# Kernel tuning notes

Measured on AMD Instinct MI355X. Metric: run time of the kernel, lower is better.

Reference implementation:

```python
import jax, jax.numpy as jnp
import numpy as np
import math

D_MODEL = 1024
D_STATE = 16
D_CONV = 4
EXPAND = 2
D_INNER = EXPAND * D_MODEL
DT_RANK = 64
BATCH = 4
SEQ_LEN = 2048


def setup_inputs() -> dict:
    key = jax.random.key(0)
    ks = jax.random.split(key, 10)
    hidden_states = jax.random.normal(ks[0], (BATCH, SEQ_LEN, D_MODEL), jnp.float32)
    in_proj_w = jax.random.normal(ks[1], (D_MODEL, 2 * D_INNER), jnp.float32) * (D_MODEL ** -0.5)
    conv_w = jax.random.normal(ks[2], (D_INNER, D_CONV), jnp.float32) * (D_CONV ** -0.5)
    conv_b = jnp.zeros((D_INNER,), jnp.float32)
    x_proj_w = jax.random.normal(ks[3], (D_INNER, DT_RANK + 2 * D_STATE), jnp.float32) * (D_INNER ** -0.5)
    dt_init_std = DT_RANK ** -0.5
    dt_proj_w = jax.random.uniform(ks[4], (DT_RANK, D_INNER), jnp.float32, -dt_init_std, dt_init_std)
    # inverse-softplus init of dt bias: dt ~ logUniform(dt_min, dt_max)
    dt_min, dt_max, dt_floor = 0.001, 0.1, 1e-4
    dt = jnp.exp(jax.random.uniform(ks[5], (D_INNER,), jnp.float32) * (math.log(dt_max) - math.log(dt_min)) + math.log(dt_min))
    dt = jnp.clip(dt, dt_floor, None)
    dt_proj_b = dt + jnp.log(-jnp.expm1(-dt))
    A = jnp.tile(jnp.arange(1, D_STATE + 1, dtype=jnp.float32)[None, :], (D_INNER, 1))
    A_log = jnp.log(A)
    D = jnp.ones((D_INNER,), jnp.float32)
    out_proj_w = jax.random.normal(ks[6], (D_INNER, D_MODEL), jnp.float32) * (D_INNER ** -0.5)
    return {
        "hidden_states": hidden_states,
        "in_proj_w": in_proj_w,
        "conv_w": conv_w,
        "conv_b": conv_b,
        "x_proj_w": x_proj_w,
        "dt_proj_w": dt_proj_w,
        "dt_proj_b": dt_proj_b,
        "A_log": A_log,
        "D": D,
        "out_proj_w": out_proj_w,
    }


def _mamba_forward(hidden_states, in_proj_w, conv_w, conv_b, x_proj_w, dt_proj_w, dt_proj_b, A_log, D, out_proj_w):
    b, L, _ = hidden_states.shape
    d_state = A_log.shape[1]
    dt_rank = dt_proj_w.shape[0]
    K = conv_w.shape[1]

    xz = hidden_states @ in_proj_w                     # (b, L, 2*d_inner)
    x, z = jnp.split(xz, 2, axis=-1)                   # each (b, L, d_inner)

    # causal depthwise conv1d (padding = K-1, truncated to L)
    x_pad = jnp.pad(x, ((0, 0), (K - 1, 0), (0, 0)))
    x = sum(x_pad[:, k:k + L, :] * conv_w[:, k] for k in range(K)) + conv_b
    x = jax.nn.silu(x)

    x_dbl = x @ x_proj_w                               # (b, L, dt_rank + 2*d_state)
    dt, B, C = jnp.split(x_dbl, [dt_rank, dt_rank + d_state], axis=-1)
    dt = jax.nn.softplus(dt @ dt_proj_w + dt_proj_b)   # (b, L, d_inner)
    A = -jnp.exp(A_log)                                # (d_inner, d_state)

    def step(h, inp):
        x_t, dt_t, B_t, C_t = inp                      # (b,d), (b,d), (b,n), (b,n)
        dA = jnp.exp(A[None] * dt_t[..., None])        # (b, d, n)
        h = dA * h + dt_t[..., None] * B_t[:, None, :] * x_t[..., None]
        y_t = jnp.einsum('bdn,bn->bd', h, C_t) + D * x_t
        return h, y_t

    h0 = jnp.zeros((b, x.shape[-1], d_state), x.dtype)
    xs = (x.transpose(1, 0, 2), dt.transpose(1, 0, 2), B.transpose(1, 0, 2), C.transpose(1, 0, 2))
    _, ys = jax.lax.scan(step, h0, xs)                 # ys: (L, b, d_inner)
    y = ys.transpose(1, 0, 2) * jax.nn.silu(z)
    return y @ out_proj_w                              # (b, L, d_model)


def reference(hidden_states, in_proj_w, conv_w, conv_b, x_proj_w, dt_proj_w, dt_proj_b, A_log, D, out_proj_w):
    return _mamba_forward(hidden_states, in_proj_w, conv_w, conv_b, x_proj_w, dt_proj_w, dt_proj_b, A_log, D, out_proj_w)
```

## Files before the change

### kernel.cpp

```cpp
#include <hip/hip_runtime.h>
#include <hip/hip_bf16.h>


#define DM 1024
#define DS 16
#define DC 4
#define DI 2048
#define DR 64
#define NB 4
#define SL 2048
#define NTOK (NB*SL)
#define XDBL_W (DR + 2*DS)
#define CONV_R 8

typedef __hip_bfloat16 bf16;
typedef unsigned short u16;
typedef __attribute__((ext_vector_type(8))) short s8v;
typedef __attribute__((ext_vector_type(4))) float f4v;
typedef __attribute__((ext_vector_type(2))) float f2v;
typedef __attribute__((ext_vector_type(4))) unsigned short us4;

__device__ __forceinline__ float b2f(bf16 v) { return __bfloat162float(v); }
__device__ __forceinline__ bf16  f2b(float v) { return __float2bfloat16(v); }
__device__ __forceinline__ u16 f2u(float x) {
    union { bf16 h; u16 s; } u; u.h = f2b(x); return u.s;
}
__device__ __forceinline__ float u2f(u16 s) {
    union { bf16 h; u16 s; } u; u.s = s; return b2f(u.h);
}

__device__ __forceinline__ bool sniff_bf16(const void* Dones) {
    return ((const u16*)Dones)[0] == 0x3F80u;
}

__device__ __forceinline__ float softplus_fast(float v) {
    return fmaxf(v, 0.f) + __logf(1.f + __expf(-fabsf(v)));
}

__device__ __forceinline__ float silu_fast(float v) {
    return v * __builtin_amdgcn_rcpf(1.f + __expf(-v));
}

template<int MODE>
__device__ __forceinline__ float ld(const void* p, size_t i, bool bf) {
    if (MODE == 0) return b2f(((const bf16*)p)[i]);
    if (MODE == 1) return ((const float*)p)[i];
    return bf ? b2f(((const bf16*)p)[i]) : ((const float*)p)[i];
}
template<int MODE>
__device__ __forceinline__ void st(void* p, size_t i, bool bf, float v) {
    if (MODE == 0)      { ((bf16*)p)[i] = f2b(v); }
    else if (MODE == 1) { ((float*)p)[i] = v; }
    else { if (bf) ((bf16*)p)[i] = f2b(v); else ((float*)p)[i] = v; }
}

template<int CM>
__device__ __forceinline__ void cstore(void* C, void* C2, size_t m, int n,
                                       int ldc, bool bf, float v) {
    if (CM == 3) {
        if (n < DR) ((bf16*)C2)[m * DR + n] = f2b(v);
        else        ((float*)C)[m * (2 * DS) + (n - DR)] = v;
    } else {
        st<CM>(C, m * (size_t)ldc + n, bf, v);
    }
}

#define AS1 __attribute__((address_space(1)))
#define AS3 __attribute__((address_space(3)))
__device__ __forceinline__ void gload_lds16(const void* g, void* l) {
    __builtin_amdgcn_global_load_lds((const AS1 unsigned int*)g,
                                     (AS3 unsigned int*)l, 16, 0, 0);
}

__global__ __launch_bounds__(256) void cast_bf16_kernel(
    const void* __restrict__ src, bf16* __restrict__ dst,
    const void* __restrict__ sniff)
{
    const bool bf = sniff_bf16(sniff);
    const size_t i = ((size_t)blockIdx.x * 256 + threadIdx.x) * 4;
    if (bf) {
        *(us4*)((u16*)dst + i) = *(const us4*)((const u16*)src + i);
    } else {
        const f4v f = *(const f4v*)((const float*)src + i);
        us4 o; o.x = f2u(f.x); o.y = f2u(f.y); o.z = f2u(f.z); o.w = f2u(f.w);
        *(us4*)((u16*)dst + i) = o;
    }
}

__global__ __launch_bounds__(256) void transpose_w(
    const void* __restrict__ w, bf16* __restrict__ wt,
    int K, int N, const void* __restrict__ sniff)
{
    const bool bf = sniff_bf16(sniff);
    __shared__ float t[32][33];
    const int tx = threadIdx.x & 31, ty = threadIdx.x >> 5;
    const int n0 = blockIdx.x * 32, k0 = blockIdx.y * 32;
    #pragma unroll
    for (int i = 0; i < 4; i++) {
        int k = k0 + ty + i * 8, n = n0 + tx;
        t[ty + i * 8][tx] = (n < N) ? ld<2>(w, (size_t)k * N + n, bf) : 0.f;
    }
    __syncthreads();
    #pragma unroll
    for (int i = 0; i < 4; i++) {
        int n = n0 + ty + i * 8, k = k0 + tx;
        wt[(size_t)n * K + k] = f2b(t[tx][ty + i * 8]);
    }
}

template<int BM, int BN, int WM, int WN, int CM, int EPI>
__global__ __launch_bounds__(WM*WN*64, 2) void gemm_big(
    const bf16* __restrict__ A, int lda,
    const bf16* __restrict__ Bt,
    void* __restrict__ C, int ldc, int K,
    const void* __restrict__ bias,
    const void* __restrict__ sniff)
{
    constexpr int NT  = WM * WN;
    constexpr int NTH = NT * 64;
    constexpr int WAVE_M = BM / WM, WAVE_N = BN / WN;
    constexpr int MR = WAVE_M / 16, NR = WAVE_N / 16, MR2 = MR / 2;
    constexpr int CH_ROWS = NTH / 8;
    constexpr int ACH = BM / CH_ROWS;
    constexpr int BCH = BN / CH_ROWS;

    const bool bf = sniff_bf16(sniff);
    __shared__ short Asm[2][BM * 64];
    __shared__ short Bsm[2][BN * 64];

    const int tid = threadIdx.x, lane = tid & 63, wave = tid >> 6;
    const int wm = wave / WN, wn = wave % WN;
    const int ll = lane & 15, qd = lane >> 4;
    const int m0 = blockIdx.x * BM, n0 = blockIdx.y * BN;

    const int s_r  = tid >> 3;
    const int s_cb = ((tid & 7) * 16) ^ ((s_r & 7) << 4);

    const char* Ab = (const char*)A;
    const char* Bb = (const char*)Bt;

    f4v acc[MR][NR];
    #pragma unroll
    for (int i = 0; i < MR; i++)
        #pragma unroll
        for (int j = 0; j < NR; j++) acc[i][j] = (f4v){0.f, 0.f, 0.f, 0.f};

    #pragma unroll
    for (int c = 0; c < ACH; c++)
        gload_lds16(Ab + (((size_t)(m0 + c * CH_ROWS + s_r) * lda) << 1) + s_cb,
                    (char*)&Asm[0][0] + (c * NTH + tid) * 16);
    #pragma unroll
    for (int c = 0; c < BCH; c++)
        gload_lds16(Bb + (((size_t)(n0 + c * CH_ROWS + s_r) * K) << 1) + s_cb,
                    (char*)&Bsm[0][0] + (c * NTH + tid) * 16);
    asm volatile("s_waitcnt vmcnt(0)" ::: "memory");
    __builtin_amdgcn_sched_barrier(0);
    __builtin_amdgcn_s_barrier();

    const int NTILE = K >> 6;
    for (int t = 0; t < NTILE; ++t) {
        const int cur = t & 1, nxt = cur ^ 1;
        const int kk = (t + 1) << 6;
        const bool more = (t + 1 < NTILE);
        const char* Ac = (const char*)&Asm[cur][0];
        const char* Bc = (const char*)&Bsm[cur][0];
        #pragma unroll
        for (int p = 0; p < 4; ++p) {
            const int kh = p >> 1, mh = p & 1;
            const int kb = kh * 64;
            s8v af[MR2], bv[NR];
            #pragma unroll
            for (int i = 0; i < MR2; i++) {
                const int row = wm * WAVE_M + (mh * MR2 + i) * 16 + ll;
                af[i] = *(const s8v*)(Ac + (size_t)row * 128
                                        + ((kb + qd * 16) ^ ((ll & 7) << 4)));
            }
            #pragma unroll
            for (int j = 0; j < NR; j++) {
                const int row = wn * WAVE_N + j * 16 + ll;
                bv[j] = *(const s8v*)(Bc + (size_t)row * 128
                                        + ((kb + qd * 16) ^ ((ll & 7) << 4)));
            }
            if (p == 0 && more) {
                #pragma unroll
                for (int c = 0; c < ACH; c++)
                    gload_lds16(Ab + (((size_t)(m0 + c * CH_ROWS + s_r) * lda + kk) << 1) + s_cb,
                                (char*)&Asm[nxt][0] + (c * NTH + tid) * 16);
            }
            if (p == 1 && more) {
                #pragma unroll
                for (int c = 0; c < BCH; c++)
                    gload_lds16(Bb + (((size_t)(n0 + c * CH_ROWS + s_r) * K + kk) << 1) + s_cb,
                                (char*)&Bsm[nxt][0] + (c * NTH + tid) * 16);
            }
            __builtin_amdgcn_sched_barrier(0);
            __builtin_amdgcn_s_barrier();
            asm volatile("s_waitcnt lgkmcnt(0)" ::: "memory");
            __builtin_amdgcn_sched_barrier(0);
            __builtin_amdgcn_s_setprio(1);
            #pragma unroll
            for (int i = 0; i < MR2; i++)
                #pragma unroll
                for (int j = 0; j < NR; j++)
                    acc[mh * MR2 + i][j] = __builtin_amdgcn_mfma_f32_16x16x32_bf16(
                        af[i], bv[j], acc[mh * MR2 + i][j], 0, 0, 0);
            __builtin_amdgcn_s_setprio(0);
            if (p == 3) {
                asm volatile("s_waitcnt vmcnt(0)" ::: "memory");
            }
            __builtin_amdgcn_sched_barrier(0);
            __builtin_amdgcn_s_barrier();
        }
    }

    #pragma unroll
    for (int j = 0; j < NR; j++) {
        const int col = n0 + wn * WAVE_N + j * 16 + ll;
        float bvv = 0.f;
        if (EPI == 1) bvv = ld<2>(bias, col, bf);
        #pragma unroll
        for (int i = 0; i < MR; i++) {
            #pragma unroll
            for (int r = 0; r < 4; r++) {
                const int row = m0 + wm * WAVE_M + i * 16 + qd * 4 + r;
                float v = acc[i][j][r];
                if (EPI == 1) v = softplus_fast(v + bvv);
                st<CM>(C, (size_t)row * ldc + col, bf, v);
            }
        }
    }
}

template<int CM, int EPI>
__global__ __launch_bounds__(256) void gemm_mfma(
    const bf16* __restrict__ A, int lda,
    const bf16* __restrict__ Bt,
    void* __restrict__ C, void* __restrict__ C2, int ldc,
    int M, int N, int K,
    const void* __restrict__ bias,
    const void* __restrict__ sniff)
{
    const bool bf = sniff_bf16(sniff);
    __shared__ short As[128 * 32];
    __shared__ short Bs[128 * 32];

    const int tid  = threadIdx.x;
    const int lane = tid & 63;
    const int wave = tid >> 6;
    const int wm = (wave & 1) * 64;
    const int wn = (wave >> 1) * 64;
    const int m0 = blockIdx.x * 128;
    const int n0 = blockIdx.y * 128;
    const int ll = lane & 15;
    const int qd = lane >> 4;

    const int srow  = lane >> 2;
    const int skoff = (lane & 3) * 8;

    const short* Ag = (const short*)A;
    const short* Bg = (const short*)Bt;
    char* AsB = (char*)As + wave * 2048 + lane * 16;
    char* BsB = (char*)Bs + wave * 2048 + lane * 16;
    const size_t a_row = (size_t)(m0 + wave * 32 + srow);
    const size_t b_row = (size_t)(n0 + wave * 32 + srow);

    f4v acc[4][4];
    #pragma unroll
    for (int i = 0; i < 4; i++)
        #pragma unroll
        for (int j = 0; j < 4; j++)
            acc[i][j] = (f4v){0.f, 0.f, 0.f, 0.f};

    for (int k0 = 0; k0 < K; k0 += 32) {
        gload_lds16(Ag + a_row * lda + k0 + skoff,            AsB);
        gload_lds16(Ag + (a_row + 16) * lda + k0 + skoff,     AsB + 1024);
        gload_lds16(Bg + b_row * K + k0 + skoff,              BsB);
        gload_lds16(Bg + (b_row + 16) * K + k0 + skoff,       BsB + 1024);
        __syncthreads();

        s8v af[4], bfr[4];
        #pragma unroll
        for (int s = 0; s < 4; s++)
            af[s] = *(const s8v*)&As[(wm + s * 16 + ll) * 32 + qd * 8];
        #pragma unroll
        for (int s = 0; s < 4; s++)
            bfr[s] = *(const s8v*)&Bs[(wn + s * 16 + ll) * 32 + qd * 8];
        #pragma unroll
        for (int i = 0; i < 4; i++)
            #pragma unroll
            for (int j = 0; j < 4; j++)
                acc[i][j] = __builtin_amdgcn_mfma_f32_16x16x32_bf16(
                    af[i], bfr[j], acc[i][j], 0, 0, 0);
        __syncthreads();
    }

    #pragma unroll
    for (int sn = 0; sn < 4; sn++) {
        const int cn = n0 + wn + sn * 16 + ll;
        if (cn >= N) continue;
        float bvv = 0.f;
        if (EPI == 1) bvv = ld<2>(bias, cn, bf);
        #pragma unroll
        for (int sm = 0; sm < 4; sm++) {
            #pragma unroll
            for (int r = 0; r < 4; r++) {
                const int cm = m0 + wm + sm * 16 + qd * 4 + r;
                float v = acc[sm][sn][r];
                if (EPI == 1) v = softplus_fast(v + bvv);
                cstore<CM>(C, C2, (size_t)cm, cn, ldc, bf, v);
            }
        }
    }
}

template<int AM, int CM, int EPI>
__global__ __launch_bounds__(256) void gemm_kernel(
    const void* __restrict__ A, int lda,
    const void* __restrict__ B, size_t bbase, int ldb,
    void* __restrict__ C, void* __restrict__ C2, int ldc,
    int M, int N, int K,
    const void* __restrict__ bias,
    const void* __restrict__ sniff)
{
    const bool bf = sniff_bf16(sniff);
    const int BM = 64, BN = 64, BK = 16;
    __shared__ float Asm[BK][BM + 4];
    __shared__ float Bsm[BK][BN + 4];

    const int tid = threadIdx.x;
    const int m0 = blockIdx.x * BM;
    const int n0 = blockIdx.y * BN;
    const int tx = tid % 16;
    const int ty = tid / 16;
    const int a_k = tid % BK;
    const int a_m = tid / BK;
    const int b_n = tid % BN;
    const int b_k = tid / BN;

    float acc[4][4] = {};

    for (int k0 = 0; k0 < K; k0 += BK) {
        #pragma unroll
        for (int i = 0; i < 4; i++) {
            int m = m0 + a_m + i * 16;
            float v = 0.f;
            if (m < M) v = ld<AM>(A, (size_t)m * lda + (k0 + a_k), bf);
            Asm[a_k][a_m + i * 16] = v;
        }
        #pragma unroll
        for (int i = 0; i < 4; i++) {
            int kk = b_k + i * 4;
            int n = n0 + b_n;
            float v = 0.f;
            if (n < N) v = ld<2>(B, bbase + (size_t)(k0 + kk) * ldb + n, bf);
            Bsm[kk][b_n] = v;
        }
        __syncthreads();
        #pragma unroll
        for (int kk = 0; kk < BK; kk++) {
            float av[4], bv[4];
            #pragma unroll
            for (int i = 0; i < 4; i++) av[i] = Asm[kk][ty * 4 + i];
            #pragma unroll
            for (int j = 0; j < 4; j++) bv[j] = Bsm[kk][tx * 4 + j];
            #pragma unroll
            for (int i = 0; i < 4; i++)
                #pragma unroll
                for (int j = 0; j < 4; j++)
                    acc[i][j] += av[i] * bv[j];
        }
        __syncthreads();
    }
    #pragma unroll
    for (int i = 0; i < 4; i++) {
        int m = m0 + ty * 4 + i;
        if (m >= M) continue;
        #pragma unroll
        for (int j = 0; j < 4; j++) {
            int n = n0 + tx * 4 + j;
            if (n >= N) continue;
            float v = acc[i][j];
            if (EPI == 1) {
                v += ld<2>(bias, n, bf);
                v = softplus_fast(v);
            }
            cstore<CM>(C, C2, (size_t)m, n, ldc, bf, v);
        }
    }
}

__global__ __launch_bounds__(256) void conv_silu_kernel(
    const bf16* __restrict__ xg, const void* __restrict__ w,
    const void* __restrict__ bias, bf16* __restrict__ xc,
    const void* __restrict__ sniff)
{
    const bool bf = sniff_bf16(sniff);
    const int c  = blockIdx.x * 256 + threadIdx.x;
    const int r0 = blockIdx.y * CONV_R;
    const int l0 = r0 % SL;

    float w0, w1, w2, w3;
    if (bf) {
        const us4 wv = *(const us4*)((const u16*)w + (size_t)c * 4);
        w0 = u2f(wv.x); w1 = u2f(wv.y); w2 = u2f(wv.z); w3 = u2f(wv.w);
    } else {
        const f4v wv = *(const f4v*)((const float*)w + (size_t)c * 4);
        w0 = wv.x; w1 = wv.y; w2 = wv.z; w3 = wv.w;
    }
    const float bs = ld<2>(bias, c, bf);

    float xm3 = (l0 >= 3) ? b2f(xg[(size_t)(r0 - 3) * DI + c]) : 0.f;
    float xm2 = (l0 >= 2) ? b2f(xg[(size_t)(r0 - 2) * DI + c]) : 0.f;
    float xm1 = (l0 >= 1) ? b2f(xg[(size_t)(r0 - 1) * DI + c]) : 0.f;

    #pragma unroll
    for (int i = 0; i < CONV_R; i++) {
        const size_t row = (size_t)(r0 + i);
        const float x0 = b2f(xg[row * DI + c]);
        const float acc = bs + w0 * xm3 + w1 * xm2 + w2 * xm1 + w3 * x0;
        const float s = acc / (1.f + __expf(-acc));
        xc[row * DI + c] = f2b(s);
        xm3 = xm2; xm2 = xm1; xm1 = x0;
    }
}

__global__ __launch_bounds__(256) void scan_pass1(
    const bf16* __restrict__ xc, const bf16* __restrict__ dt,
    const float* __restrict__ bc,
    const void* __restrict__ A_log, const void* __restrict__ Dones,
    float* __restrict__ P, float* __restrict__ Q, int nch)
{
    const bool bf = sniff_bf16(Dones);
    const int tid = threadIdx.x;
    const int d = blockIdx.x * 256 + tid;
    const int c = blockIdx.y;
    const int b = blockIdx.z;
    const int T = SL / nch;
    __shared__ u16 xs[32 * 256];
    __shared__ u16 ts[32 * 256];
    __shared__ float bcs[32 * 2 * DS];

    const size_t base = (size_t)b * SL + (size_t)c * T;
    const int lane = tid & 63, wv = tid >> 6;
    const int d0 = blockIdx.x * 256;
    const u16* xg16 = (const u16*)xc + base * DI + d0;
    const u16* tg16 = (const u16*)dt + base * DI + d0;
    for (int k = wv; k < (T >> 1); k += 4) {
        const int row = (k << 1) + (lane >> 5);
        const int c8  = (lane & 31) * 8;
        gload_lds16(xg16 + (size_t)row * DI + c8, (char*)xs + k * 1024 + lane * 16);
        gload_lds16(tg16 + (size_t)row * DI + c8, (char*)ts + k * 1024 + lane * 16);
    }
    const u16* bc16 = (const u16*)(bc + base * (2 * DS));
    for (int k = wv; k < (T >> 3); k += 4)
        gload_lds16(bc16 + k * 512 + lane * 8, (char*)bcs + k * 1024 + lane * 16);

    float a[DS];
    bool lad = true;
    #pragma unroll
    for (int n = 0; n < DS; n++) {
        a[n] = -__expf(ld<2>(A_log, (size_t)d * DS + n, bf));
        lad = lad && (fabsf(a[n] - (n + 1) * a[0]) < 1e-3f);
    }
    __syncthreads();

    float Pp[DS], Qq[DS];
    if (lad) {
        const float a0 = a[0];
        float R = 1.f;
        f2v q2[8];
        #pragma unroll
        for (int j = 0; j < 8; j++) q2[j] = (f2v){0.f, 0.f};
        for (int i = 0; i < T; i++) {
            const float xv = u2f(xs[i * 256 + tid]);
            const float tv = u2f(ts[i * 256 + tid]);
            const float dtx = tv * xv;
            const f4v* B4 = (const f4v*)&bcs[i * 2 * DS];
            const float r = __expf(a0 * tv);
            const float r2 = r * r, r4 = r2 * r2;
            const f2v r4v = {r4, r4};
            f2v cA = {r, r2};
            f2v cB = {r2 * r, r4};
            const f2v dtx2 = {dtx, dtx};
            R *= r;
            #pragma unroll
            for (int j4 = 0; j4 < 4; j4++) {
                const f4v Bq = B4[j4];
                const f2v b0 = {Bq.x, Bq.y}, b1 = {Bq.z, Bq.w};
                q2[2 * j4]     = cA * q2[2 * j4]     + dtx2 * b0;
                q2[2 * j4 + 1] = cB * q2[2 * j4 + 1] + dtx2 * b1;
                cA *= r4v; cB *= r4v;
            }
        }
        const float R2 = R * R, R3 = R2 * R, R4 = R2 * R2;
        float pa = R, pb = R2, pc = R3, pd = R4;
        #pragma unroll
        for (int n = 0; n < DS; n += 4) {
            Pp[n] = pa; Pp[n + 1] = pb; Pp[n + 2] = pc; Pp[n + 3] = pd;
            pa *= R4; pb *= R4; pc *= R4; pd *= R4;
        }
        #pragma unroll
        for (int j = 0; j < 8; j++) { Qq[2 * j] = q2[j].x; Qq[2 * j + 1] = q2[j].y; }
    } else {
        #pragma unroll
        for (int n = 0; n < DS; n++) { Pp[n] = 1.f; Qq[n] = 0.f; }
        for (int i = 0; i < T; i++) {
            const float xv = u2f(xs[i * 256 + tid]);
            const float tv = u2f(ts[i * 256 + tid]);
            const float dtx = tv * xv;
            const float* Bv = &bcs[i * 2 * DS];
            #pragma unroll
            for (int n = 0; n < DS; n++) {
                const float dA = __expf(a[n] * tv);
                Pp[n] *= dA;
                Qq[n] = dA * Qq[n] + dtx * Bv[n];
            }
        }
    }
    const size_t ob = ((size_t)b * nch + c) * (DS * DI) + d;
    #pragma unroll
    for (int n = 0; n < DS; n++) {
        P[ob + (size_t)n * DI] = Pp[n];
        Q[ob + (size_t)n * DI] = Qq[n];
    }
}

__global__ __launch_bounds__(256) void scan_pass2(
    float* __restrict__ P, const float* __restrict__ Q, int nch)
{
    const int j = blockIdx.x * 256 + threadIdx.x;
    const int b = blockIdx.y;
    float h = 0.f;
    for (int c = 0; c < nch; c++) {
        const size_t o = ((size_t)b * nch + c) * (DI * DS) + j;
        const float p = P[o];
        const float q = Q[o];
        P[o] = h;
        h = p * h + q;
    }
}

__global__ __launch_bounds__(256) void scan_pass3(
    const bf16* __restrict__ xc, const bf16* __restrict__ dt,
    const float* __restrict__ bc, bf16* __restrict__ z,
    const void* __restrict__ A_log, const void* __restrict__ Dones,
    const float* __restrict__ H, int nch)
{
    const bool bf = sniff_bf16(Dones);
    const int tid = threadIdx.x;
    const int d = blockIdx.x * 256 + tid;
    const int c = blockIdx.y;
    const int b = blockIdx.z;
    const int T = SL / nch;
    __shared__ u16 xs[32 * 256];
    __shared__ u16 ts[32 * 256];
    __shared__ u16 zs[32 * 256];
    __shared__ float bcs[32 * 2 * DS];

    const size_t base = (size_t)b * SL + (size_t)c * T;
    const int lane = tid & 63, wv = tid >> 6;
    const int d0 = blockIdx.x * 256;
    const u16* xg16 = (const u16*)xc + base * DI + d0;
    const u16* tg16 = (const u16*)dt + base * DI + d0;
    const u16* zg16 = (const u16*)z + base * DI + d0;
    for (int k = wv; k < (T >> 1); k += 4) {
        const int row = (k << 1) + (lane >> 5);
        const int c8  = (lane & 31) * 8;
        gload_lds16(xg16 + (size_t)row * DI + c8, (char*)xs + k * 1024 + lane * 16);
        gload_lds16(tg16 + (size_t)row * DI + c8, (char*)ts + k * 1024 + lane * 16);
        gload_lds16(zg16 + (size_t)row * DI + c8, (char*)zs + k * 1024 + lane * 16);
    }
    const u16* bc16 = (const u16*)(bc + base * (2 * DS));
    for (int k = wv; k < (T >> 3); k += 4)
        gload_lds16(bc16 + k * 512 + lane * 8, (char*)bcs + k * 1024 + lane * 16);

    float a[DS];
    bool lad = true;
    const size_t ob = ((size_t)b * nch + c) * (DS * DI) + d;
    #pragma unroll
    for (int n = 0; n < DS; n++) {
        a[n] = -__expf(ld<2>(A_log, (size_t)d * DS + n, bf));
        lad = lad && (fabsf(a[n] - (n + 1) * a[0]) < 1e-3f);
    }
    const float dD = ld<2>(Dones, d, bf);
    u16* zp = (u16*)z + base * DI + d;
    __syncthreads();

    if (lad) {
        const float a0 = a[0];
        f2v h2[8];
        #pragma unroll
        for (int j = 0; j < 8; j++)
            h2[j] = (f2v){H[ob + (size_t)(2 * j) * DI],
                          H[ob + (size_t)(2 * j + 1) * DI]};
        for (int i = 0; i < T; i++) {
            const float xv = u2f(xs[i * 256 + tid]);
            const float tv = u2f(ts[i * 256 + tid]);
            const float zv = u2f(zs[i * 256 + tid]);
            const float dtx = tv * xv;
            const f4v* B4 = (const f4v*)&bcs[i * 2 * DS];
            const f4v* C4 = B4 + 4;
            const float r = __expf(a0 * tv);
            const float r2 = r * r, r4 = r2 * r2;
            const f2v r4v = {r4, r4};
            f2v cA = {r, r2};
            f2v cB = {r2 * r, r4};
            const f2v dtx2 = {dtx, dtx};
            f2v ya = {dD * xv, 0.f}, yb = {0.f, 0.f};
            #pragma unroll
            for (int j4 = 0; j4 < 4; j4++) {
                const f4v Bq = B4[j4], Cq = C4[j4];
                const f2v b0 = {Bq.x, Bq.y}, b1 = {Bq.z, Bq.w};
                const f2v c0 = {Cq.x, Cq.y}, c1 = {Cq.z, Cq.w};
                h2[2 * j4]     = cA * h2[2 * j4]     + dtx2 * b0;
                ya += h2[2 * j4] * c0;
                h2[2 * j4 + 1] = cB * h2[2 * j4 + 1] + dtx2 * b1;
                yb += h2[2 * j4 + 1] * c1;
                cA *= r4v; cB *= r4v;
            }
            const float y = (ya.x + ya.y) + (yb.x + yb.y);
            zp[(size_t)i * DI] = f2u(y * silu_fast(zv));
        }
    } else {
        float h[DS];
        #pragma unroll
        for (int n = 0; n < DS; n++) h[n] = H[ob + (size_t)n * DI];
        for (int i = 0; i < T; i++) {
            const float xv = u2f(xs[i * 256 + tid]);
            const float tv = u2f(ts[i * 256 + tid]);
            const float zv = u2f(zs[i * 256 + tid]);
            const float dtx = tv * xv;
            const float* Bv = &bcs[i * 2 * DS];
            const float* Cv = Bv + DS;
            float y = dD * xv;
            #pragma unroll
            for (int n = 0; n < DS; n++) {
                const float dA = __expf(a[n] * tv);
                h[n] = dA * h[n] + dtx * Bv[n];
                y += h[n] * Cv[n];
            }
            zp[(size_t)i * DI] = f2u(y * silu_fast(zv));
        }
    }
}

__global__ __launch_bounds__(256) void scan_serial(
    const bf16* __restrict__ xc, const bf16* __restrict__ dt,
    const float* __restrict__ bc, bf16* __restrict__ z,
    const void* __restrict__ A_log, const void* __restrict__ Dones)
{
    const bool bf = sniff_bf16(Dones);
    const int d = blockIdx.x * 256 + threadIdx.x;
    const int b = blockIdx.y;
    float a[DS], h[DS];
    #pragma unroll
    for (int n = 0; n < DS; n++) {
        a[n] = -__expf(ld<2>(A_log, (size_t)d * DS + n, bf));
        h[n] = 0.f;
    }
    const float dD = ld<2>(Dones, d, bf);
    const size_t base = (size_t)b * SL;
    for (int l = 0; l < SL; l++) {
        const size_t row = base + l;
        const float xv  = b2f(xc[row * DI + d]);
        const float dtv = b2f(dt[row * DI + d]);
        const float* Bv = bc + row * (2 * DS);
        const float dtx = dtv * xv;
        float y = dD * xv;
        #pragma unroll
        for (int n = 0; n < DS; n++) {
            const float dA = __expf(a[n] * dtv);
            h[n] = dA * h[n] + dtx * Bv[n];
            y += h[n] * Bv[DS + n];
        }
        const float zv = b2f(z[row * DI + d]);
        const float g = zv / (1.f + __expf(-zv));
        z[row * DI + d] = f2b(y * g);
    }
}

extern "C" void kernel_launch(void* const* d_in, const int* in_sizes, int n_in,
                              void* d_out, int out_size, void* d_ws, size_t ws_size,
                              hipStream_t stream) {
    const void* hs        = d_in[0];
    const void* in_proj_w = d_in[1];
    const void* conv_w    = d_in[2];
    const void* conv_b    = d_in[3];
    const void* x_proj_w  = d_in[4];
    const void* dt_proj_w = d_in[5];
    const void* dt_proj_b = d_in[6];
    const void* A_log     = d_in[7];
    const void* Dones     = d_in[8];
    const void* out_proj_w= d_in[9];

    char* ws = (char*)d_ws;
    bf16*  xg   = (bf16*)(ws);
    bf16*  xc   = (bf16*)(ws + 33554432);
    bf16*  hsb  = (bf16*)(ws + 33554432);
    bf16*  z    = (bf16*)(ws + 67108864);
    float* bc   = (float*)(ws + 100663296);
    bf16*  dtf  = (bf16*)(ws + 101711872);
    const size_t WT_OFF = 102760448;
    bf16* in_projT  = (bf16*)(ws + WT_OFF);
    bf16* x_projT   = (bf16*)(ws + WT_OFF);
    bf16* dt_projT  = (bf16*)(ws + WT_OFF + 524288);
    bf16* out_projT = (bf16*)(ws + WT_OFF);
    const bool mfma_ok = ws_size >= WT_OFF + 8388608;

    const size_t per_chunk = (size_t)NB * DI * DS * 4 * 2;
    int nch = 64;
    while (nch > 1 && WT_OFF + (size_t)nch * per_chunk > ws_size) nch >>= 1;
    const bool chunked = (nch >= 64) &&
                         (WT_OFF + (size_t)nch * per_chunk <= ws_size);
    float* P = (float*)(ws + WT_OFF);
    float* Q = P + (size_t)NB * nch * DI * DS;

    bf16* dtb = xg;

    if (mfma_ok) {
        cast_bf16_kernel<<<(NTOK*DM/4)/256, 256, 0, stream>>>(hs, hsb, Dones);
        transpose_w<<<dim3((2*DI)/32, DM/32), 256, 0, stream>>>(
            in_proj_w, in_projT, DM, 2*DI, Dones);
        gemm_big<256, 256, 2, 4, 0, 0><<<dim3(NTOK/256, DI/256), 512, 0, stream>>>(
            hsb, DM, in_projT, xg, DI, DM, nullptr, Dones);
        gemm_big<256, 256, 2, 4, 0, 0><<<dim3(NTOK/256, DI/256), 512, 0, stream>>>(
            hsb, DM, in_projT + (size_t)DI * DM, z, DI, DM, nullptr, Dones);
        conv_silu_kernel<<<dim3(DI/256, NTOK/CONV_R), 256, 0, stream>>>(
            xg, conv_w, conv_b, xc, Dones);
        transpose_w<<<dim3(128/32, DI/32), 256, 0, stream>>>(
            x_proj_w, x_projT, DI, XDBL_W, Dones);
        gemm_mfma<3, 0><<<dim3(NTOK/128, 1), 256, 0, stream>>>(
            xc, DI, x_projT, bc, dtf, 0, NTOK, XDBL_W, DI, nullptr, Dones);
        transpose_w<<<dim3(DI/32, DR/32), 256, 0, stream>>>(
            dt_proj_w, dt_projT, DR, DI, Dones);
        gemm_big<256, 128, 4, 2, 0, 1><<<dim3(NTOK/256, DI/128), 512, 0, stream>>>(
            dtf, DR, dt_projT, dtb, DI, DR, dt_proj_b, Dones);
    } else {
        gemm_kernel<2, 0, 0><<<dim3(NTOK/64, DI/64), 256, 0, stream>>>(
            hs, DM, in_proj_w, 0, 2*DI, xg, nullptr, DI, NTOK, DI, DM, nullptr, Dones);
        gemm_kernel<2, 0, 0><<<dim3(NTOK/64, DI/64), 256, 0, stream>>>(
            hs, DM, in_proj_w, DI, 2*DI, z, nullptr, DI, NTOK, DI, DM, nullptr, Dones);
        conv_silu_kernel<<<dim3(DI/256, NTOK/CONV_R), 256, 0, stream>>>(
            xg, conv_w, conv_b, xc, Dones);
        gemm_kernel<0, 3, 0><<<dim3(NTOK/64, (XDBL_W + 63)/64), 256, 0, stream>>>(
            xc, DI, x_proj_w, 0, XDBL_W, bc, dtf, 0, NTOK, XDBL_W, DI, nullptr, Dones);
        gemm_kernel<0, 0, 1><<<dim3(NTOK/64, DI/64), 256, 0, stream>>>(
            dtf, DR, dt_proj_w, 0, DI, dtb, nullptr, DI, NTOK, DI, DR, dt_proj_b, Dones);
    }

    if (chunked) {
        scan_pass1<<<dim3(DI/256, nch, NB), 256, 0, stream>>>(
            xc, dtb, bc, A_log, Dones, P, Q, nch);
        scan_pass2<<<dim3((DI*DS)/256, NB), 256, 0, stream>>>(P, Q, nch);
        scan_pass3<<<dim3(DI/256, nch, NB), 256, 0, stream>>>(
            xc, dtb, bc, z, A_log, Dones, P, nch);
    } else {
        scan_serial<<<dim3(DI/256, NB), 256, 0, stream>>>(
            xc, dtb, bc, z, A_log, Dones);
    }

    if (mfma_ok) {
        transpose_w<<<dim3(DM/32, DI/32), 256, 0, stream>>>(
            out_proj_w, out_projT, DI, DM, Dones);
        gemm_big<256, 128, 4, 2, 2, 0><<<dim3(NTOK/256, DM/128), 512, 0, stream>>>(
            z, DI, out_projT, d_out, DM, DI, nullptr, Dones);
    } else {
        gemm_kernel<0, 2, 0><<<dim3(NTOK/64, DM/64), 256, 0, stream>>>(
            z, DI, out_proj_w, 0, DM, d_out, nullptr, DM, NTOK, DM, DI, nullptr, Dones);
    }
}
```

Before: 448.4 us.

## Merge in_proj GEMMs into one launch and split-K the x_proj GEMM

The two in_proj GEMMs for x and z become a single gemm_big launch over the full 2*DI output width, with a new epilogue mode that routes each column to xg or z. The skinny x_proj GEMM (N=96, K=2048), which had only 64 blocks, is split along K into 4 chunks to give 256 blocks, with fp32 partials written to workspace and summed by a separate reduce kernel that writes dtf and bc. This is meant to raise GPU occupancy on the low-parallelism GEMM and remove one launch. The cost is an extra 16 MB of partial traffic and an extra kernel launch.

Measured after the change: 423.9 us. -5.5%, faster.

```diff
diff --git a/kernel.cpp b/kernel.cpp
--- a/kernel.cpp
+++ b/kernel.cpp
@@ -112,7 +112,7 @@
 __global__ __launch_bounds__(WM*WN*64, 2) void gemm_big(
     const bf16* __restrict__ A, int lda,
     const bf16* __restrict__ Bt,
-    void* __restrict__ C, int ldc, int K,
+    void* __restrict__ C, void* __restrict__ C2, int ldc, int K,
     const void* __restrict__ bias,
     const void* __restrict__ sniff)
 {
@@ -225,10 +225,102 @@
                 const int row = m0 + wm * WAVE_M + i * 16 + qd * 4 + r;
                 float v = acc[i][j][r];
                 if (EPI == 1) v = softplus_fast(v + bvv);
-                st<CM>(C, (size_t)row * ldc + col, bf, v);
-            }
-        }
-    }
+                if constexpr (CM == 4) {
+                    if (col < DI) ((bf16*)C)[(size_t)row * DI + col] = f2b(v);
+                    else          ((bf16*)C2)[(size_t)row * DI + (col - DI)] = f2b(v);
+                } else {
+                    st<CM>(C, (size_t)row * ldc + col, bf, v);
+                }
+            }
+        }
+    }
+}
+
+__global__ __launch_bounds__(256) void gemm_mfma_sk(
+    const bf16* __restrict__ A, int lda,
+    const bf16* __restrict__ Bt,
+    float* __restrict__ Cp, int M, int K, int kchunk,
+    const void* __restrict__ sniff)
+{
+    __shared__ short As[128 * 32];
+    __shared__ short Bs[128 * 32];
+
+    const int tid  = threadIdx.x;
+    const int lane = tid & 63;
+    const int wave = tid >> 6;
+    const int wm = (wave & 1) * 64;
+    const int wn = (wave >> 1) * 64;
+    const int m0 = blockIdx.x * 128;
+    const int ll = lane & 15;
+    const int qd = lane >> 4;
+    const int kbase = blockIdx.z * kchunk;
+
+    const int srow  = lane >> 2;
+    const int skoff = (lane & 3) * 8;
+
+    const short* Ag = (const short*)A;
+    const short* Bg = (const short*)Bt;
+    char* AsB = (char*)As + wave * 2048 + lane * 16;
+    char* BsB = (char*)Bs + wave * 2048 + lane * 16;
+    const size_t a_row = (size_t)(m0 + wave * 32 + srow);
+    const size_t b_row = (size_t)(wave * 32 + srow);
+
+    f4v acc[4][4];
+    #pragma unroll
+    for (int i = 0; i < 4; i++)
+        #pragma unroll
+        for (int j = 0; j < 4; j++)
+            acc[i][j] = (f4v){0.f, 0.f, 0.f, 0.f};
+
+    for (int k0 = kbase; k0 < kbase + kchunk; k0 += 32) {
+        gload_lds16(Ag + a_row * lda + k0 + skoff,            AsB);
+        gload_lds16(Ag + (a_row + 16) * lda + k0 + skoff,     AsB + 1024);
+        gload_lds16(Bg + b_row * K + k0 + skoff,              BsB);
+        gload_lds16(Bg + (b_row + 16) * K + k0 + skoff,       BsB + 1024);
+        __syncthreads();
+
+        s8v af[4], bfr[4];
+        #pragma unroll
+        for (int s = 0; s < 4; s++)
+            af[s] = *(const s8v*)&As[(wm + s * 16 + ll) * 32 + qd * 8];
+        #pragma unroll
+        for (int s = 0; s < 4; s++)
+            bfr[s] = *(const s8v*)&Bs[(wn + s * 16 + ll) * 32 + qd * 8];
+        #pragma unroll
+        for (int i = 0; i < 4; i++)
+            #pragma unroll
+            for (int j = 0; j < 4; j++)
+                acc[i][j] = __builtin_amdgcn_mfma_f32_16x16x32_bf16(
+                    af[i], bfr[j], acc[i][j], 0, 0, 0);
+        __syncthreads();
+    }
+
+    float* Co = Cp + (size_t)blockIdx.z * M * 128;
+    #pragma unroll
+    for (int sn = 0; sn < 4; sn++) {
+        const int cn = wn + sn * 16 + ll;
+        #pragma unroll
+        for (int sm = 0; sm < 4; sm++) {
+            #pragma unroll
+            for (int r = 0; r < 4; r++) {
+                const int cm = m0 + wm + sm * 16 + qd * 4 + r;
+                Co[(size_t)cm * 128 + cn] = acc[sm][sn][r];
+            }
+        }
+    }
+}
+
+__global__ __launch_bounds__(256) void g3_reduce(
+    const float* __restrict__ Cp, float* __restrict__ bc,
+    bf16* __restrict__ dtf, int nchunks)
+{
+    const int idx = blockIdx.x * 256 + threadIdx.x;
+    const int m = idx >> 7, n = idx & 127;
+    float v = 0.f;
+    for (int c = 0; c < nchunks; c++)
+        v += Cp[(size_t)c * NTOK * 128 + idx];
+    if (n < DR) dtf[(size_t)m * DR + n] = f2b(v);
+    else if (n < XDBL_W) bc[(size_t)m * (2 * DS) + (n - DR)] = v;
 }
 
 template<int CM, int EPI>
@@ -705,7 +797,9 @@
     bf16* x_projT   = (bf16*)(ws + WT_OFF);
     bf16* dt_projT  = (bf16*)(ws + WT_OFF + 524288);
     bf16* out_projT = (bf16*)(ws + WT_OFF);
+    float* g3p      = (float*)(ws + WT_OFF + 1048576);
     const bool mfma_ok = ws_size >= WT_OFF + 8388608;
+    const bool g3sk = ws_size >= WT_OFF + 1048576 + 16777216;
 
     const size_t per_chunk = (size_t)NB * DI * DS * 4 * 2;
     int nch = 64;
@@ -721,20 +815,24 @@
         cast_bf16_kernel<<<(NTOK*DM/4)/256, 256, 0, stream>>>(hs, hsb, Dones);
         transpose_w<<<dim3((2*DI)/32, DM/32), 256, 0, stream>>>(
             in_proj_w, in_projT, DM, 2*DI, Dones);
-        gemm_big<256, 256, 2, 4, 0, 0><<<dim3(NTOK/256, DI/256), 512, 0, stream>>>(
-            hsb, DM, in_projT, xg, DI, DM, nullptr, Dones);
-        gemm_big<256, 256, 2, 4, 0, 0><<<dim3(NTOK/256, DI/256), 512, 0, stream>>>(
-            hsb, DM, in_projT + (size_t)DI * DM, z, DI, DM, nullptr, Dones);
+        gemm_big<256, 256, 2, 4, 4, 0><<<dim3(NTOK/256, (2*DI)/256), 512, 0, stream>>>(
+            hsb, DM, in_projT, xg, z, DI, DM, nullptr, Dones);
         conv_silu_kernel<<<dim3(DI/256, NTOK/CONV_R), 256, 0, stream>>>(
             xg, conv_w, conv_b, xc, Dones);
         transpose_w<<<dim3(128/32, DI/32), 256, 0, stream>>>(
             x_proj_w, x_projT, DI, XDBL_W, Dones);
-        gemm_mfma<3, 0><<<dim3(NTOK/128, 1), 256, 0, stream>>>(
-            xc, DI, x_projT, bc, dtf, 0, NTOK, XDBL_W, DI, nullptr, Dones);
+        if (g3sk) {
+            gemm_mfma_sk<<<dim3(NTOK/128, 1, 4), 256, 0, stream>>>(
+                xc, DI, x_projT, g3p, NTOK, DI, 512, Dones);
+            g3_reduce<<<(NTOK*128)/256, 256, 0, stream>>>(g3p, bc, dtf, 4);
+        } else {
+            gemm_mfma<3, 0><<<dim3(NTOK/128, 1), 256, 0, stream>>>(
+                xc, DI, x_projT, bc, dtf, 0, NTOK, XDBL_W, DI, nullptr, Dones);
+        }
         transpose_w<<<dim3(DI/32, DR/32), 256, 0, stream>>>(
             dt_proj_w, dt_projT, DR, DI, Dones);
         gemm_big<256, 128, 4, 2, 0, 1><<<dim3(NTOK/256, DI/128), 512, 0, stream>>>(
-            dtf, DR, dt_projT, dtb, DI, DR, dt_proj_b, Dones);
+            dtf, DR, dt_projT, dtb, nullptr, DI, DR, dt_proj_b, Dones);
     } else {
         gemm_kernel<2, 0, 0><<<dim3(NTOK/64, DI/64), 256, 0, stream>>>(
             hs, DM, in_proj_w, 0, 2*DI, xg, nullptr, DI, NTOK, DI, DM, nullptr, Dones);
@@ -763,7 +861,7 @@
         transpose_w<<<dim3(DM/32, DI/32), 256, 0, stream>>>(
             out_proj_w, out_projT, DI, DM, Dones);
         gemm_big<256, 128, 4, 2, 2, 0><<<dim3(NTOK/256, DM/128), 512, 0, stream>>>(
-            z, DI, out_projT, d_out, DM, DI, nullptr, Dones);
+            z, DI, out_projT, d_out, nullptr, DM, DI, nullptr, Dones);
     } else {
         gemm_kernel<0, 2, 0><<<dim3(NTOK/64, DM/64), 256, 0, stream>>>(
             z, DI, out_proj_w, 0, DM, d_out, nullptr, DM, NTOK, DM, DI, nullptr, Dones);
```
